# Optimization experiments

Measured on AMD Instinct MI355X. Metric: run time of the kernel, lower is better.

The kernel has to match this reference:

```python
import jax, jax.numpy as jnp
import numpy as np

B, T, C = 2, 2048, 2048
NH, NKV = 16, 4
HD = C // NH  # 128


def _rope(x, cos, sin):
    d = x.shape[-1] // 2
    x1, x2 = x[..., :d], x[..., d:]
    return jnp.concatenate([x1 * cos + x2 * sin, -x1 * sin + x2 * cos], axis=-1)


def _rmsnorm(x):
    eps = jnp.finfo(x.dtype).eps
    return x * jax.lax.rsqrt(jnp.mean(jnp.square(x), axis=-1, keepdims=True) + eps)


def setup_inputs() -> dict:
    key = jax.random.key(0)
    ks = jax.random.split(key, 7)
    s = 0.02
    return {
        "x": jax.random.normal(ks[0], (B, T, C), jnp.float32),
        "cos": jax.random.normal(ks[1], (1, T, 1, HD // 2), jnp.float32),
        "sin": jax.random.normal(ks[2], (1, T, 1, HD // 2), jnp.float32),
        "wq": jax.random.normal(ks[3], (C, NH * HD), jnp.float32) * s,
        "wk": jax.random.normal(ks[4], (C, NKV * HD), jnp.float32) * s,
        "wv": jax.random.normal(ks[5], (C, NKV * HD), jnp.float32) * s,
        "wo": jax.random.normal(ks[6], (C, C), jnp.float32) * s,
    }


def reference(x, cos, sin, wq, wk, wv, wo):
    q = (x @ wq).reshape(B, T, NH, HD)
    k = (x @ wk).reshape(B, T, NKV, HD)
    v = (x @ wv).reshape(B, T, NKV, HD)
    q = _rmsnorm(_rope(q, cos, sin))
    k = _rmsnorm(_rope(k, cos, sin))
    # [B, H, T, D]
    q = q.transpose(0, 2, 1, 3)
    k = k.transpose(0, 2, 1, 3)
    v = v.transpose(0, 2, 1, 3)
    rep = NH // NKV
    k = jnp.repeat(k, rep, axis=1)
    v = jnp.repeat(v, rep, axis=1)
    scale = 1.0 / jnp.sqrt(jnp.float32(HD))
    scores = jnp.einsum("bhqd,bhkd->bhqk", q, k) * scale
    causal = jnp.tril(jnp.ones((T, T), bool))
    scores = jnp.where(causal, scores, jnp.finfo(scores.dtype).min)
    attn = jax.nn.softmax(scores, axis=-1)
    y = jnp.einsum("bhqk,bhkd->bhqd", attn, v)
    y = y.transpose(0, 2, 1, 3).reshape(B, T, C)
    return y @ wo
```

## Files before the change

### kernel.cpp

```cpp
#include <hip/hip_runtime.h>
#include <hip/hip_bf16.h>
#include <cstdint>

typedef unsigned short u16;
typedef __bf16 bf16x8 __attribute__((ext_vector_type(8)));
typedef float f32x4 __attribute__((ext_vector_type(4)));
typedef unsigned short u16x4 __attribute__((ext_vector_type(4)));
typedef unsigned short u16x8 __attribute__((ext_vector_type(8)));
typedef unsigned uint2v __attribute__((ext_vector_type(2)));

#define B_ 2
#define T_ 2048
#define C_ 2048
#define NH_ 16
#define NKV_ 4
#define HD_ 128
#define K2_ 0.12752004650581538f

__device__ __forceinline__ u16 f2bf(float f) {
    unsigned u = __builtin_bit_cast(unsigned, f);
    unsigned r = u + 0x7FFFu + ((u >> 16) & 1u);
    return (u16)(r >> 16);
}

__device__ __forceinline__ float bf2f(u16 v) {
    unsigned u = ((unsigned)v) << 16;
    return __builtin_bit_cast(float, u);
}

__device__ __forceinline__ unsigned cvtpk(float a, float b) {
    unsigned r;
    asm("v_cvt_pk_bf16_f32 %0, %1, %2" : "=v"(r) : "v"(a), "v"(b));
    return r;
}

__device__ __forceinline__ void gl16(const void* g, void* l) {
    auto gp = reinterpret_cast<const __attribute__((address_space(1))) unsigned*>(
        reinterpret_cast<uintptr_t>(g));
    auto lp = reinterpret_cast<__attribute__((address_space(3))) unsigned*>(
        reinterpret_cast<uintptr_t>(l));
    __builtin_amdgcn_global_load_lds(gp, lp, 16, 0, 0);
}

__global__ void transpose_conv(const float* __restrict__ in, u16* __restrict__ out, int N) {
    __shared__ float tile[32][33];
    int n0 = blockIdx.x * 32, k0 = blockIdx.y * 32;
    int tx = threadIdx.x, ty = threadIdx.y;
#pragma unroll
    for (int i = 0; i < 4; ++i)
        tile[ty * 4 + i][tx] = in[(size_t)(k0 + ty * 4 + i) * N + n0 + tx];
    __syncthreads();
#pragma unroll
    for (int i = 0; i < 4; ++i)
        out[(size_t)(n0 + ty * 4 + i) * 2048 + k0 + tx] = f2bf(tile[tx][ty * 4 + i]);
}

__global__ void convert4(const float4* __restrict__ in, u16* __restrict__ out) {
    int i = blockIdx.x * 256 + threadIdx.x;
    float4 v = in[i];
    u16x4 o;
    o[0] = f2bf(v.x); o[1] = f2bf(v.y); o[2] = f2bf(v.z); o[3] = f2bf(v.w);
    ((u16x4*)out)[i] = o;
}

__global__ __launch_bounds__(256, 2) void gemm_bf16(const u16* __restrict__ A,
                                                    const u16* __restrict__ BT,
                                                    float* __restrict__ C, int N, int K) {
    __shared__ __align__(16) u16 As[2][128 * 64];
    __shared__ __align__(16) u16 Bs[2][128 * 64];
    int nwg = gridDim.x * gridDim.y;
    int bid = blockIdx.y * gridDim.x + blockIdx.x;
    int nb = (bid & 7) * (nwg >> 3) + (bid >> 3);
    int bx = nb % gridDim.x, by = nb / gridDim.x;

    int t = threadIdx.x;
    int w = t >> 6, l = t & 63;
    int wr = w >> 1, wc = w & 1;
    int lg = l >> 4, lr = l & 15;
    int m0 = by * 128, n0 = bx * 128;
    f32x4 acc[4][4] = {};

    size_t goff[4];
#pragma unroll
    for (int i = 0; i < 4; ++i) {
        int g = t + i * 256;
        goff[i] = (size_t)(g >> 3) * K * 2 + (size_t)(((g & 7) ^ ((g >> 3) & 7)) * 16);
    }
    const char* Ab = (const char*)A + (size_t)m0 * K * 2;
    const char* Bb = (const char*)BT + (size_t)n0 * K * 2;

    auto stage = [&](int kt, int buf) {
        char* Ad = (char*)As[buf] + t * 16;
        char* Bd = (char*)Bs[buf] + t * 16;
#pragma unroll
        for (int i = 0; i < 4; ++i) {
            gl16(Ab + (size_t)kt * 2 + goff[i], Ad + i * 4096);
            gl16(Bb + (size_t)kt * 2 + goff[i], Bd + i * 4096);
        }
    };

    stage(0, 0);
    int nk = K >> 6;
    for (int ki = 0; ki < nk; ++ki) {
        asm volatile("s_waitcnt vmcnt(0)" ::: "memory");
        __builtin_amdgcn_s_barrier();
        __builtin_amdgcn_sched_barrier(0);
        int cur = ki & 1;
        if (ki + 1 < nk) stage((ki + 1) * 64, cur ^ 1);
#pragma unroll
        for (int kk = 0; kk < 2; ++kk) {
            bf16x8 af[4], bfr[4];
#pragma unroll
            for (int m = 0; m < 4; ++m)
                af[m] = *(const bf16x8*)&As[cur][(wr * 64 + m * 16 + lr) * 64 +
                                                (((kk * 4 + lg) ^ (lr & 7)) * 8)];
#pragma unroll
            for (int n = 0; n < 4; ++n)
                bfr[n] = *(const bf16x8*)&Bs[cur][(wc * 64 + n * 16 + lr) * 64 +
                                                 (((kk * 4 + lg) ^ (lr & 7)) * 8)];
#pragma unroll
            for (int m = 0; m < 4; ++m)
#pragma unroll
                for (int n = 0; n < 4; ++n)
                    acc[m][n] = __builtin_amdgcn_mfma_f32_16x16x32_bf16(af[m], bfr[n], acc[m][n], 0, 0, 0);
        }
    }
#pragma unroll
    for (int m = 0; m < 4; ++m) {
        int row = m0 + wr * 64 + m * 16 + lg * 4;
#pragma unroll
        for (int n = 0; n < 4; ++n) {
            int col = n0 + wc * 64 + n * 16 + lr;
            float* Cp = C + (size_t)row * N + col;
#pragma unroll
            for (int r = 0; r < 4; ++r)
                Cp[(size_t)r * N] = acc[m][n][r];
        }
    }
}

__global__ __launch_bounds__(256, 2) void gemm_bf16o(const u16* __restrict__ A,
                                                     const u16* __restrict__ BT,
                                                     u16* __restrict__ C, int N, int K) {
    __shared__ __align__(16) u16 As[2][128 * 64];
    __shared__ __align__(16) u16 Bs[2][128 * 64];
    int nwg = gridDim.x * gridDim.y;
    int bid = blockIdx.y * gridDim.x + blockIdx.x;
    int nb = (bid & 7) * (nwg >> 3) + (bid >> 3);
    int bx = nb % gridDim.x, by = nb / gridDim.x;

    int t = threadIdx.x;
    int w = t >> 6, l = t & 63;
    int wr = w >> 1, wc = w & 1;
    int lg = l >> 4, lr = l & 15;
    int m0 = by * 128, n0 = bx * 128;
    f32x4 acc[4][4] = {};

    size_t goff[4];
#pragma unroll
    for (int i = 0; i < 4; ++i) {
        int g = t + i * 256;
        goff[i] = (size_t)(g >> 3) * K * 2 + (size_t)(((g & 7) ^ ((g >> 3) & 7)) * 16);
    }
    const char* Ab = (const char*)A + (size_t)m0 * K * 2;
    const char* Bb = (const char*)BT + (size_t)n0 * K * 2;

    auto stage = [&](int kt, int buf) {
        char* Ad = (char*)As[buf] + t * 16;
        char* Bd = (char*)Bs[buf] + t * 16;
#pragma unroll
        for (int i = 0; i < 4; ++i) {
            gl16(Ab + (size_t)kt * 2 + goff[i], Ad + i * 4096);
            gl16(Bb + (size_t)kt * 2 + goff[i], Bd + i * 4096);
        }
    };

    stage(0, 0);
    int nk = K >> 6;
    for (int ki = 0; ki < nk; ++ki) {
        asm volatile("s_waitcnt vmcnt(0)" ::: "memory");
        __builtin_amdgcn_s_barrier();
        __builtin_amdgcn_sched_barrier(0);
        int cur = ki & 1;
        if (ki + 1 < nk) stage((ki + 1) * 64, cur ^ 1);
#pragma unroll
        for (int kk = 0; kk < 2; ++kk) {
            bf16x8 af[4], bfr[4];
#pragma unroll
            for (int m = 0; m < 4; ++m)
                af[m] = *(const bf16x8*)&As[cur][(wr * 64 + m * 16 + lr) * 64 +
                                                (((kk * 4 + lg) ^ (lr & 7)) * 8)];
#pragma unroll
            for (int n = 0; n < 4; ++n)
                bfr[n] = *(const bf16x8*)&Bs[cur][(wc * 64 + n * 16 + lr) * 64 +
                                                 (((kk * 4 + lg) ^ (lr & 7)) * 8)];
#pragma unroll
            for (int m = 0; m < 4; ++m)
#pragma unroll
                for (int n = 0; n < 4; ++n)
                    acc[m][n] = __builtin_amdgcn_mfma_f32_16x16x32_bf16(af[m], bfr[n], acc[m][n], 0, 0, 0);
        }
    }
#pragma unroll
    for (int m = 0; m < 4; ++m) {
        int row = m0 + wr * 64 + m * 16 + lg * 4;
#pragma unroll
        for (int n = 0; n < 4; ++n) {
            int col = n0 + wc * 64 + n * 16 + lr;
            u16* Cp = C + (size_t)row * N + col;
#pragma unroll
            for (int r = 0; r < 4; ++r)
                Cp[(size_t)r * N] = f2bf(acc[m][n][r]);
        }
    }
}

__global__ void rope_rms(const u16* __restrict__ qkv, const float* __restrict__ cs,
                         const float* __restrict__ sn, u16* __restrict__ qh,
                         u16* __restrict__ kh) {
    int task = blockIdx.x * 4 + (threadIdx.x >> 6);
    int l = threadIdx.x & 63;
    const u16* in;
    u16* out;
    int tpos;
    float post = 1.0f;
    if (task < 65536) {
        int row = task >> 4, h = task & 15;
        in = qkv + (size_t)row * 3072 + h * 128;
        int b = row >> 11; tpos = row & 2047;
        out = qh + ((size_t)(b * NH_ + h) * T_ + tpos) * HD_;
        post = K2_;
    } else {
        int t2 = task - 65536;
        int row = t2 >> 2, h = t2 & 3;
        in = qkv + (size_t)row * 3072 + 2048 + h * 128;
        int b = row >> 11; tpos = row & 2047;
        out = kh + ((size_t)(b * NKV_ + h) * T_ + tpos) * HD_;
    }
    float x1 = bf2f(in[l]), x2 = bf2f(in[l + 64]);
    float c = cs[tpos * 64 + l], s = sn[tpos * 64 + l];
    float o1 = x1 * c + x2 * s;
    float o2 = -x1 * s + x2 * c;
    float ss = o1 * o1 + o2 * o2;
#pragma unroll
    for (int m = 1; m < 64; m <<= 1) ss += __shfl_xor(ss, m);
    float r = rsqrtf(ss * (1.0f / 128.0f) + 1.1920929e-07f) * post;
    out[l] = f2bf(o1 * r);
    out[l + 64] = f2bf(o2 * r);
}

__global__ void transpose_v(const u16* __restrict__ qkv, u16* __restrict__ vt) {
    __shared__ u16 tile[32][34];
    int t0 = blockIdx.x * 32;
    int d0 = blockIdx.y * 32;
    int bk = blockIdx.z;
    int b = bk >> 2, kvh = bk & 3;
    int tx = threadIdx.x, ty = threadIdx.y;
#pragma unroll
    for (int i = 0; i < 4; ++i)
        tile[ty * 4 + i][tx] =
            qkv[(size_t)(b * 2048 + t0 + ty * 4 + i) * 3072 + 2560 + kvh * 128 + d0 + tx];
    __syncthreads();
#pragma unroll
    for (int i = 0; i < 4; ++i)
        vt[((size_t)bk * 128 + d0 + ty * 4 + i) * 2048 + t0 + tx] = tile[tx][ty * 4 + i];
}

__global__ __launch_bounds__(256, 2) void attn(const u16* __restrict__ Q,
                                               const u16* __restrict__ Kk,
                                               const u16* __restrict__ V,
                                               u16* __restrict__ Y,
                                               u16* __restrict__ Opart,
                                               float2* __restrict__ Ml) {
    extern __shared__ __align__(16) u16 sm[];
    u16* Ks = sm;
    u16* Vs = sm + 16384;
    u16* Pb = sm + 24576;

    int bid = blockIdx.x;
    int xcd = bid & 7;
    int b = xcd >> 2, kvh = xcd & 3;
    int tidx = bid >> 3;
    int j, g0, g1, seg;
    bool split;
    if (tidx < 32) {
        j = tidx; g0 = 0; g1 = (j >> 1) + 1; split = false; seg = 0;
    } else if (tidx < 64) {
        j = 95 - tidx; int NNs = (j >> 1) + 1;
        g0 = 0; g1 = NNs >> 1; split = true; seg = 0;
    } else {
        j = 127 - tidx; int NNs = (j >> 1) + 1;
        g0 = NNs >> 1; g1 = NNs; split = true; seg = 1;
    }
    int t = threadIdx.x;
    int w = t >> 6, l = t & 63;
    int lg = l >> 4, lr = l & 15;
    int h = kvh * 4 + w;
    int qw = j * 32;

    const u16* Qp = Q + (size_t)(b * NH_ + h) * T_ * HD_;
    const u16* Kp = Kk + (size_t)(b * NKV_ + kvh) * T_ * HD_;
    const u16* Vp = V + (size_t)(b * NKV_ + kvh) * HD_ * T_;
    u16* Yp = Y + (size_t)(b * T_) * 2048 + h * HD_;
    u16* Pw = Pb + w * 512;

    size_t koff[4], voff[4];
#pragma unroll
    for (int i = 0; i < 4; ++i) {
        int g = t + i * 256;
        koff[i] = (size_t)(g >> 4) * 256 + (size_t)(((g & 15) ^ ((g >> 4) & 15)) * 16);
        voff[i] = (size_t)(g >> 3) * (T_ * 2) + (size_t)(((g & 7) ^ ((g >> 3) & 7)) * 16);
    }
    auto stageK = [&](int kv0, int buf) {
        const char* Kb = (const char*)Kp + (size_t)kv0 * 256;
        char* Kd = (char*)Ks + buf * 16384 + t * 16;
#pragma unroll
        for (int i = 0; i < 4; ++i) gl16(Kb + koff[i], Kd + i * 4096);
    };
    auto stageV = [&](int kv0) {
        const char* Vb = (const char*)Vp + (size_t)kv0 * 2;
        char* Vd = (char*)Vs + t * 16;
#pragma unroll
        for (int i = 0; i < 4; ++i) gl16(Vb + voff[i], Vd + i * 4096);
    };

    bf16x8 aq[2][4];
#pragma unroll
    for (int qf = 0; qf < 2; ++qf)
#pragma unroll
        for (int ch = 0; ch < 4; ++ch)
            aq[qf][ch] = *(const bf16x8*)(Qp + (size_t)(qw + qf * 16 + lr) * HD_ + ch * 32 + lg * 8);

    f32x4 acc[2][8] = {};
    float m2[2] = {-1e30f, -1e30f};
    float lp_[2] = {0.0f, 0.0f};

    stageK(g0 * 64, 0);

    for (int gi = g0; gi < g1; ++gi) {
        asm volatile("s_waitcnt vmcnt(0)" ::: "memory");
        __builtin_amdgcn_s_barrier();
        __builtin_amdgcn_sched_barrier(0);
        int cur = (gi - g0) & 1;
        int kv0 = gi * 64;
        stageV(kv0);
        __builtin_amdgcn_sched_barrier(0);
        int gn = (gi + 1 < g1) ? gi + 1 : g0;
        stageK(gn * 64, cur ^ 1);
        __builtin_amdgcn_sched_barrier(0);
        int kbase = cur * 8192;

        f32x4 sc[2][4] = {};
        __builtin_amdgcn_s_setprio(1);
#pragma unroll
        for (int ch = 0; ch < 4; ++ch)
#pragma unroll
            for (int kf = 0; kf < 4; ++kf) {
                bf16x8 bk = *(const bf16x8*)&Ks[kbase + (kf * 16 + lr) * 128 + (((ch * 4 + lg) ^ lr) * 8)];
                sc[0][kf] = __builtin_amdgcn_mfma_f32_16x16x32_bf16(bk, aq[0][ch], sc[0][kf], 0, 0, 0);
                sc[1][kf] = __builtin_amdgcn_mfma_f32_16x16x32_bf16(bk, aq[1][ch], sc[1][kf], 0, 0, 0);
            }
        __builtin_amdgcn_s_setprio(0);

        if (kv0 + 63 > qw) {
#pragma unroll
            for (int qf = 0; qf < 2; ++qf) {
                int qrow = qw + qf * 16 + lr;
#pragma unroll
                for (int kf = 0; kf < 4; ++kf)
#pragma unroll
                    for (int r = 0; r < 4; ++r) {
                        int key = kv0 + kf * 16 + 4 * lg + r;
                        if (key > qrow) sc[qf][kf][r] = -1e38f;
                    }
            }
        }
        float mx[2];
#pragma unroll
        for (int qf = 0; qf < 2; ++qf) {
            float m = sc[qf][0][0];
#pragma unroll
            for (int kf = 0; kf < 4; ++kf)
#pragma unroll
                for (int r = 0; r < 4; ++r) m = fmaxf(m, sc[qf][kf][r]);
            m = fmaxf(m, __shfl_xor(m, 16));
            m = fmaxf(m, __shfl_xor(m, 32));
            mx[qf] = m;
        }
        bool upd = (mx[0] > m2[0] + 8.0f) || (mx[1] > m2[1] + 8.0f);
        if (__any(upd)) {
#pragma unroll
            for (int qf = 0; qf < 2; ++qf) {
                float mn = fmaxf(m2[qf], mx[qf]);
                float rs = exp2f(m2[qf] - mn);
                m2[qf] = mn;
                lp_[qf] *= rs;
                float rs4[4];
#pragma unroll
                for (int r = 0; r < 4; ++r) rs4[r] = __shfl(rs, 4 * lg + r, 16);
#pragma unroll
                for (int oc = 0; oc < 8; ++oc)
#pragma unroll
                    for (int r = 0; r < 4; ++r) acc[qf][oc][r] *= rs4[r];
            }
        }
        bf16x8 ap[2][2];
#pragma unroll
        for (int kk = 0; kk < 2; ++kk) {
#pragma unroll
            for (int qf = 0; qf < 2; ++qf) {
                float ps = 0.0f;
#pragma unroll
                for (int kfl = 0; kfl < 2; ++kfl) {
                    int kf = kk * 2 + kfl;
                    float p0 = exp2f(sc[qf][kf][0] - m2[qf]);
                    float p1 = exp2f(sc[qf][kf][1] - m2[qf]);
                    float p2 = exp2f(sc[qf][kf][2] - m2[qf]);
                    float p3 = exp2f(sc[qf][kf][3] - m2[qf]);
                    ps += (p0 + p1) + (p2 + p3);
                    uint2v pk;
                    pk[0] = cvtpk(p0, p1);
                    pk[1] = cvtpk(p2, p3);
                    int g = 2 * kfl + (lg >> 1);
                    *(uint2v*)&Pw[lr * 32 + ((g ^ (lr & 3)) * 8) + (lg & 1) * 4] = pk;
                }
                lp_[qf] += ps;
                ap[qf][kk] = *(const bf16x8*)&Pw[lr * 32 + ((lg ^ (lr & 3)) * 8)];
            }
        }
        asm volatile("s_waitcnt vmcnt(4)" ::: "memory");
        __builtin_amdgcn_s_barrier();
        __builtin_amdgcn_sched_barrier(0);

        __builtin_amdgcn_s_setprio(1);
#pragma unroll
        for (int oc = 0; oc < 8; ++oc)
#pragma unroll
            for (int kk = 0; kk < 2; ++kk) {
                bf16x8 bv = *(const bf16x8*)&Vs[(oc * 16 + lr) * 64 +
                                                (((kk * 4 + lg) ^ (lr & 7)) * 8)];
                acc[0][oc] = __builtin_amdgcn_mfma_f32_16x16x32_bf16(ap[0][kk], bv, acc[0][oc], 0, 0, 0);
                acc[1][oc] = __builtin_amdgcn_mfma_f32_16x16x32_bf16(ap[1][kk], bv, acc[1][oc], 0, 0, 0);
            }
        __builtin_amdgcn_s_setprio(0);
    }
    asm volatile("s_waitcnt vmcnt(0)" ::: "memory");

    float ltr[2];
#pragma unroll
    for (int qf = 0; qf < 2; ++qf) {
        float lt = lp_[qf];
        lt += __shfl_xor(lt, 16);
        lt += __shfl_xor(lt, 32);
        ltr[qf] = lt;
    }

    if (!split) {
#pragma unroll
        for (int qf = 0; qf < 2; ++qf) {
            float inv = 1.0f / ltr[qf];
            float inv4[4];
#pragma unroll
            for (int r = 0; r < 4; ++r) inv4[r] = __shfl(inv, 4 * lg + r, 16);
#pragma unroll
            for (int oc = 0; oc < 8; ++oc)
#pragma unroll
                for (int r = 0; r < 4; ++r)
                    Yp[(size_t)(qw + qf * 16 + 4 * lg + r) * 2048 + oc * 16 + lr] =
                        f2bf(acc[qf][oc][r] * inv4[r]);
        }
    } else {
        int s32 = j - 32;
        size_t pbase = (((size_t)(xcd * 32 + s32) * 2 + seg) * 4 + w);
        u16* Op = Opart + pbase * 4096;
        float2* mlp = Ml + pbase * 32;
#pragma unroll
        for (int qf = 0; qf < 2; ++qf)
#pragma unroll
            for (int oc = 0; oc < 8; ++oc)
#pragma unroll
                for (int r = 0; r < 4; ++r)
                    Op[(qf * 16 + 4 * lg + r) * 128 + oc * 16 + lr] = f2bf(acc[qf][oc][r]);
        if (lg == 0) {
            mlp[lr] = float2{m2[0], ltr[0]};
            mlp[16 + lr] = float2{m2[1], ltr[1]};
        }
    }
}

__global__ __launch_bounds__(256) void combine(const u16* __restrict__ Opart,
                                               const float2* __restrict__ Ml,
                                               u16* __restrict__ Y) {
    int blk = blockIdx.x;
    int w = blk & 3;
    int s32 = (blk >> 2) & 31;
    int xcd = blk >> 7;
    int b = xcd >> 2, kvh = xcd & 3, h = kvh * 4 + w;
    int qw = (32 + s32) * 32;
    size_t p0 = (((size_t)(xcd * 32 + s32) * 2 + 0) * 4 + w);
    size_t p1 = (((size_t)(xcd * 32 + s32) * 2 + 1) * 4 + w);
    int t = threadIdx.x;
    int row = t >> 3, c0 = (t & 7) * 16;
    float2 a = Ml[p0 * 32 + row];
    float2 c = Ml[p1 * 32 + row];
    float M = fmaxf(a.x, c.x);
    float w1 = exp2f(a.x - M), w2 = exp2f(c.x - M);
    float inv = 1.0f / (w1 * a.y + w2 * c.y);
    const u16* O1 = Opart + p0 * 4096 + row * 128 + c0;
    const u16* O2 = Opart + p1 * 4096 + row * 128 + c0;
    u16* Yp = Y + ((size_t)(b * T_) + qw + row) * 2048 + h * HD_ + c0;
    u16x8 v1a = *(const u16x8*)O1, v1b = *(const u16x8*)(O1 + 8);
    u16x8 v2a = *(const u16x8*)O2, v2b = *(const u16x8*)(O2 + 8);
    u16x8 oa, ob;
#pragma unroll
    for (int i = 0; i < 8; ++i) {
        oa[i] = f2bf((w1 * bf2f(v1a[i]) + w2 * bf2f(v2a[i])) * inv);
        ob[i] = f2bf((w1 * bf2f(v1b[i]) + w2 * bf2f(v2b[i])) * inv);
    }
    *(u16x8*)Yp = oa;
    *(u16x8*)(Yp + 8) = ob;
}

extern "C" void kernel_launch(void* const* d_in, const int* in_sizes, int n_in,
                              void* d_out, int out_size, void* d_ws, size_t ws_size,
                              hipStream_t stream) {
    const float* x    = (const float*)d_in[0];
    const float* cosT = (const float*)d_in[1];
    const float* sinT = (const float*)d_in[2];
    const float* wq   = (const float*)d_in[3];
    const float* wk   = (const float*)d_in[4];
    const float* wv   = (const float*)d_in[5];
    const float* wo   = (const float*)d_in[6];
    float* out = (float*)d_out;

    char* ws = (char*)d_ws;
    u16*    wqkvT = (u16*)(ws);
    u16*    woT   = (u16*)(ws + 12582912);
    u16*    xb    = (u16*)(ws + 20971520);
    u16*    qkv   = (u16*)(ws + 37748736);
    u16*    opart = (u16*)(ws + 62914560);
    float2* mlbuf = (float2*)(ws + 79691776);
    u16*    qh    = (u16*)(ws + 88080384);
    u16*    kh    = (u16*)(ws + 104857600);
    u16*    vt    = (u16*)(ws + 109051904);
    u16*    y     = xb;

    hipFuncSetAttribute(reinterpret_cast<const void*>(&attn),
                        hipFuncAttributeMaxDynamicSharedMemorySize, 53248);

    transpose_conv<<<dim3(64, 64), dim3(32, 8), 0, stream>>>(wq, wqkvT, 2048);
    transpose_conv<<<dim3(16, 64), dim3(32, 8), 0, stream>>>(wk, wqkvT + (size_t)2048 * 2048, 512);
    transpose_conv<<<dim3(16, 64), dim3(32, 8), 0, stream>>>(wv, wqkvT + (size_t)2560 * 2048, 512);
    transpose_conv<<<dim3(64, 64), dim3(32, 8), 0, stream>>>(wo, woT, 2048);
    convert4<<<8192, 256, 0, stream>>>((const float4*)x, xb);

    gemm_bf16o<<<dim3(24, 32), 256, 0, stream>>>(xb, wqkvT, qkv, 3072, 2048);

    rope_rms<<<20480, 256, 0, stream>>>(qkv, cosT, sinT, qh, kh);
    transpose_v<<<dim3(64, 4, 8), dim3(32, 8), 0, stream>>>(qkv, vt);

    attn<<<768, 256, 53248, stream>>>(qh, kh, vt, y, opart, mlbuf);
    combine<<<1024, 256, 0, stream>>>(opart, mlbuf, y);

    gemm_bf16<<<dim3(16, 32), 256, 0, stream>>>(y, woT, out, 2048, 2048);
}
```

Before: 201.9 us.

## Widen attention blocks to 512 threads covering 64 query rows per KV tile

The attention kernel now uses 8 waves per block, two query sub-tiles of 32 rows for each of the 4 heads. Each staged K/V tile is therefore shared by twice as many queries, which halves the global-to-LDS traffic per query. The split-KV schedule and the combine kernel are remapped to match: 16 unsplit tiles, 32 split halves, and combine reading 64-row partials. In exchange, occupancy drops to one block per CU, with larger blocks, fewer of them, and coarser load balancing.

```diff
diff --git a/kernel.cpp b/kernel.cpp
--- a/kernel.cpp
+++ b/kernel.cpp
@@ -266,7 +266,7 @@
         vt[((size_t)bk * 128 + d0 + ty * 4 + i) * 2048 + t0 + tx] = tile[tx][ty * 4 + i];
 }
 
-__global__ __launch_bounds__(256, 2) void attn(const u16* __restrict__ Q,
+__global__ __launch_bounds__(512, 1) void attn(const u16* __restrict__ Q,
                                                const u16* __restrict__ Kk,
                                                const u16* __restrict__ V,
                                                u16* __restrict__ Y,
@@ -280,23 +280,22 @@
     int bid = blockIdx.x;
     int xcd = bid & 7;
     int b = xcd >> 2, kvh = xcd & 3;
-    int tidx = bid >> 3;
+    int tk = bid >> 3;
     int j, g0, g1, seg;
     bool split;
-    if (tidx < 32) {
-        j = tidx; g0 = 0; g1 = (j >> 1) + 1; split = false; seg = 0;
-    } else if (tidx < 64) {
-        j = 95 - tidx; int NNs = (j >> 1) + 1;
-        g0 = 0; g1 = NNs >> 1; split = true; seg = 0;
+    if (tk < 16) {
+        j = tk; g0 = 0; g1 = j + 1; split = false; seg = 0;
+    } else if (tk < 32) {
+        j = tk; g0 = 0; g1 = 16; split = true; seg = 0;
     } else {
-        j = 127 - tidx; int NNs = (j >> 1) + 1;
-        g0 = NNs >> 1; g1 = NNs; split = true; seg = 1;
+        j = 63 - tk; g0 = 16; g1 = j + 1; split = true; seg = 1;
     }
     int t = threadIdx.x;
     int w = t >> 6, l = t & 63;
     int lg = l >> 4, lr = l & 15;
-    int h = kvh * 4 + w;
-    int qw = j * 32;
+    int hh = w & 3;
+    int h = kvh * 4 + hh;
+    int qw = j * 64 + (w >> 2) * 32;
 
     const u16* Qp = Q + (size_t)(b * NH_ + h) * T_ * HD_;
     const u16* Kp = Kk + (size_t)(b * NKV_ + kvh) * T_ * HD_;
@@ -304,10 +303,10 @@
     u16* Yp = Y + (size_t)(b * T_) * 2048 + h * HD_;
     u16* Pw = Pb + w * 512;
 
-    size_t koff[4], voff[4];
-#pragma unroll
-    for (int i = 0; i < 4; ++i) {
-        int g = t + i * 256;
+    size_t koff[2], voff[2];
+#pragma unroll
+    for (int i = 0; i < 2; ++i) {
+        int g = t + i * 512;
         koff[i] = (size_t)(g >> 4) * 256 + (size_t)(((g & 15) ^ ((g >> 4) & 15)) * 16);
         voff[i] = (size_t)(g >> 3) * (T_ * 2) + (size_t)(((g & 7) ^ ((g >> 3) & 7)) * 16);
     }
@@ -315,13 +314,13 @@
         const char* Kb = (const char*)Kp + (size_t)kv0 * 256;
         char* Kd = (char*)Ks + buf * 16384 + t * 16;
 #pragma unroll
-        for (int i = 0; i < 4; ++i) gl16(Kb + koff[i], Kd + i * 4096);
+        for (int i = 0; i < 2; ++i) gl16(Kb + koff[i], Kd + i * 8192);
     };
     auto stageV = [&](int kv0) {
         const char* Vb = (const char*)Vp + (size_t)kv0 * 2;
         char* Vd = (char*)Vs + t * 16;
 #pragma unroll
-        for (int i = 0; i < 4; ++i) gl16(Vb + voff[i], Vd + i * 4096);
+        for (int i = 0; i < 2; ++i) gl16(Vb + voff[i], Vd + i * 8192);
     };
 
     bf16x8 aq[2][4];
@@ -428,7 +427,7 @@
                 ap[qf][kk] = *(const bf16x8*)&Pw[lr * 32 + ((lg ^ (lr & 3)) * 8)];
             }
         }
-        asm volatile("s_waitcnt vmcnt(4)" ::: "memory");
+        asm volatile("s_waitcnt vmcnt(2)" ::: "memory");
         __builtin_amdgcn_s_barrier();
         __builtin_amdgcn_sched_barrier(0);
 
@@ -470,20 +469,21 @@
                         f2bf(acc[qf][oc][r] * inv4[r]);
         }
     } else {
-        int s32 = j - 32;
-        size_t pbase = (((size_t)(xcd * 32 + s32) * 2 + seg) * 4 + w);
-        u16* Op = Opart + pbase * 4096;
-        float2* mlp = Ml + pbase * 32;
+        int s16 = j - 16;
+        size_t pbase = (((size_t)(xcd * 16 + s16) * 4 + hh) * 2 + seg);
+        u16* Op = Opart + pbase * 8192;
+        float2* mlp = Ml + pbase * 64;
+        int ro = (w >> 2) * 32;
 #pragma unroll
         for (int qf = 0; qf < 2; ++qf)
 #pragma unroll
             for (int oc = 0; oc < 8; ++oc)
 #pragma unroll
                 for (int r = 0; r < 4; ++r)
-                    Op[(qf * 16 + 4 * lg + r) * 128 + oc * 16 + lr] = f2bf(acc[qf][oc][r]);
+                    Op[(ro + qf * 16 + 4 * lg + r) * 128 + oc * 16 + lr] = f2bf(acc[qf][oc][r]);
         if (lg == 0) {
-            mlp[lr] = float2{m2[0], ltr[0]};
-            mlp[16 + lr] = float2{m2[1], ltr[1]};
+            mlp[ro + lr] = float2{m2[0], ltr[0]};
+            mlp[ro + 16 + lr] = float2{m2[1], ltr[1]};
         }
     }
 }
@@ -492,33 +492,33 @@
                                                const float2* __restrict__ Ml,
                                                u16* __restrict__ Y) {
     int blk = blockIdx.x;
-    int w = blk & 3;
-    int s32 = (blk >> 2) & 31;
-    int xcd = blk >> 7;
-    int b = xcd >> 2, kvh = xcd & 3, h = kvh * 4 + w;
-    int qw = (32 + s32) * 32;
-    size_t p0 = (((size_t)(xcd * 32 + s32) * 2 + 0) * 4 + w);
-    size_t p1 = (((size_t)(xcd * 32 + s32) * 2 + 1) * 4 + w);
+    int hh = blk & 3;
+    int s16 = (blk >> 2) & 15;
+    int xcd = blk >> 6;
+    int b = xcd >> 2, kvh = xcd & 3, h = kvh * 4 + hh;
+    size_t p0 = (size_t)blk * 2;
+    size_t p1 = p0 + 1;
     int t = threadIdx.x;
-    int row = t >> 3, c0 = (t & 7) * 16;
-    float2 a = Ml[p0 * 32 + row];
-    float2 c = Ml[p1 * 32 + row];
+    int row = t >> 2, c0 = (t & 3) * 32;
+    float2 a = Ml[p0 * 64 + row];
+    float2 c = Ml[p1 * 64 + row];
     float M = fmaxf(a.x, c.x);
     float w1 = exp2f(a.x - M), w2 = exp2f(c.x - M);
     float inv = 1.0f / (w1 * a.y + w2 * c.y);
-    const u16* O1 = Opart + p0 * 4096 + row * 128 + c0;
-    const u16* O2 = Opart + p1 * 4096 + row * 128 + c0;
-    u16* Yp = Y + ((size_t)(b * T_) + qw + row) * 2048 + h * HD_ + c0;
-    u16x8 v1a = *(const u16x8*)O1, v1b = *(const u16x8*)(O1 + 8);
-    u16x8 v2a = *(const u16x8*)O2, v2b = *(const u16x8*)(O2 + 8);
-    u16x8 oa, ob;
-#pragma unroll
-    for (int i = 0; i < 8; ++i) {
-        oa[i] = f2bf((w1 * bf2f(v1a[i]) + w2 * bf2f(v2a[i])) * inv);
-        ob[i] = f2bf((w1 * bf2f(v1b[i]) + w2 * bf2f(v2b[i])) * inv);
-    }
-    *(u16x8*)Yp = oa;
-    *(u16x8*)(Yp + 8) = ob;
+    const u16* O1 = Opart + p0 * 8192 + row * 128 + c0;
+    const u16* O2 = Opart + p1 * 8192 + row * 128 + c0;
+    int qrow = (16 + s16) * 64 + row;
+    u16* Yp = Y + ((size_t)(b * T_) + qrow) * 2048 + h * HD_ + c0;
+#pragma unroll
+    for (int v = 0; v < 4; ++v) {
+        u16x8 v1 = *(const u16x8*)(O1 + v * 8);
+        u16x8 v2 = *(const u16x8*)(O2 + v * 8);
+        u16x8 o;
+#pragma unroll
+        for (int i = 0; i < 8; ++i)
+            o[i] = f2bf((w1 * bf2f(v1[i]) + w2 * bf2f(v2[i])) * inv);
+        *(u16x8*)(Yp + v * 8) = o;
+    }
 }
 
 extern "C" void kernel_launch(void* const* d_in, const int* in_sizes, int n_in,
@@ -546,7 +546,7 @@
     u16*    y     = xb;
 
     hipFuncSetAttribute(reinterpret_cast<const void*>(&attn),
-                        hipFuncAttributeMaxDynamicSharedMemorySize, 53248);
+                        hipFuncAttributeMaxDynamicSharedMemorySize, 57344);
 
     transpose_conv<<<dim3(64, 64), dim3(32, 8), 0, stream>>>(wq, wqkvT, 2048);
     transpose_conv<<<dim3(16, 64), dim3(32, 8), 0, stream>>>(wk, wqkvT + (size_t)2048 * 2048, 512);
@@ -559,8 +559,8 @@
     rope_rms<<<20480, 256, 0, stream>>>(qkv, cosT, sinT, qh, kh);
     transpose_v<<<dim3(64, 4, 8), dim3(32, 8), 0, stream>>>(qkv, vt);
 
-    attn<<<768, 256, 53248, stream>>>(qh, kh, vt, y, opart, mlbuf);
-    combine<<<1024, 256, 0, stream>>>(opart, mlbuf, y);
+    attn<<<384, 512, 57344, stream>>>(qh, kh, vt, y, opart, mlbuf);
+    combine<<<512, 256, 0, stream>>>(opart, mlbuf, y);
 
     gemm_bf16<<<dim3(16, 32), 256, 0, stream>>>(y, woT, out, 2048, 2048);
 }
```

Result: no change. 200.9 us (-0.5%).

## Merge prep kernels and single-buffer attention K/V to fit three blocks per CU

Applied to the files above, without the earlier changes.

Folds the four weight transpose-converts and the x conversion into one prepass launch, and rope_rms with transpose_v into one launch, which cuts kernel launch count. In attention, K staging drops from double to single buffering, shrinking LDS from 52KB to 36KB so launch bounds can rise to three blocks per CU. K and V are now loaded together at the top of each iteration and waited on in full, so load latency is no longer prefetched behind compute and must be hidden by the extra occupancy instead.

```diff
diff --git a/kernel.cpp b/kernel.cpp
--- a/kernel.cpp
+++ b/kernel.cpp
@@ -42,10 +42,34 @@
     __builtin_amdgcn_global_load_lds(gp, lp, 16, 0, 0);
 }
 
-__global__ void transpose_conv(const float* __restrict__ in, u16* __restrict__ out, int N) {
+__global__ __launch_bounds__(256) void prepass(const float* __restrict__ wq,
+                                               const float* __restrict__ wk,
+                                               const float* __restrict__ wv,
+                                               const float* __restrict__ wo,
+                                               const float4* __restrict__ x,
+                                               u16* __restrict__ wqkvT,
+                                               u16* __restrict__ woT,
+                                               u16* __restrict__ xb) {
+    int bz = blockIdx.x;
+    int t = threadIdx.x;
+    if (bz >= 10240) {
+        int i = (bz - 10240) * 256 + t;
+        float4 v = x[i];
+        u16x4 o;
+        o[0] = f2bf(v.x); o[1] = f2bf(v.y); o[2] = f2bf(v.z); o[3] = f2bf(v.w);
+        ((u16x4*)xb)[i] = o;
+        return;
+    }
     __shared__ float tile[32][33];
-    int n0 = blockIdx.x * 32, k0 = blockIdx.y * 32;
-    int tx = threadIdx.x, ty = threadIdx.y;
+    const float* in;
+    u16* out;
+    int N, bx, by;
+    if (bz < 4096)      { in = wq; out = wqkvT;                      N = 2048; bx = bz & 63; by = bz >> 6; }
+    else if (bz < 5120) { int z = bz - 4096; in = wk; out = wqkvT + (size_t)2048 * 2048; N = 512; bx = z & 15; by = z >> 4; }
+    else if (bz < 6144) { int z = bz - 5120; in = wv; out = wqkvT + (size_t)2560 * 2048; N = 512; bx = z & 15; by = z >> 4; }
+    else                { int z = bz - 6144; in = wo; out = woT;     N = 2048; bx = z & 63; by = z >> 6; }
+    int n0 = bx * 32, k0 = by * 32;
+    int tx = t & 31, ty = t >> 5;
 #pragma unroll
     for (int i = 0; i < 4; ++i)
         tile[ty * 4 + i][tx] = in[(size_t)(k0 + ty * 4 + i) * N + n0 + tx];
@@ -53,14 +77,6 @@
 #pragma unroll
     for (int i = 0; i < 4; ++i)
         out[(size_t)(n0 + ty * 4 + i) * 2048 + k0 + tx] = f2bf(tile[tx][ty * 4 + i]);
-}
-
-__global__ void convert4(const float4* __restrict__ in, u16* __restrict__ out) {
-    int i = blockIdx.x * 256 + threadIdx.x;
-    float4 v = in[i];
-    u16x4 o;
-    o[0] = f2bf(v.x); o[1] = f2bf(v.y); o[2] = f2bf(v.z); o[3] = f2bf(v.w);
-    ((u16x4*)out)[i] = o;
 }
 
 __global__ __launch_bounds__(256, 2) void gemm_bf16(const u16* __restrict__ A,
@@ -215,47 +231,52 @@
     }
 }
 
-__global__ void rope_rms(const u16* __restrict__ qkv, const float* __restrict__ cs,
-                         const float* __restrict__ sn, u16* __restrict__ qh,
-                         u16* __restrict__ kh) {
-    int task = blockIdx.x * 4 + (threadIdx.x >> 6);
-    int l = threadIdx.x & 63;
-    const u16* in;
-    u16* out;
-    int tpos;
-    float post = 1.0f;
-    if (task < 65536) {
-        int row = task >> 4, h = task & 15;
-        in = qkv + (size_t)row * 3072 + h * 128;
-        int b = row >> 11; tpos = row & 2047;
-        out = qh + ((size_t)(b * NH_ + h) * T_ + tpos) * HD_;
-        post = K2_;
-    } else {
-        int t2 = task - 65536;
-        int row = t2 >> 2, h = t2 & 3;
-        in = qkv + (size_t)row * 3072 + 2048 + h * 128;
-        int b = row >> 11; tpos = row & 2047;
-        out = kh + ((size_t)(b * NKV_ + h) * T_ + tpos) * HD_;
-    }
-    float x1 = bf2f(in[l]), x2 = bf2f(in[l + 64]);
-    float c = cs[tpos * 64 + l], s = sn[tpos * 64 + l];
-    float o1 = x1 * c + x2 * s;
-    float o2 = -x1 * s + x2 * c;
-    float ss = o1 * o1 + o2 * o2;
-#pragma unroll
-    for (int m = 1; m < 64; m <<= 1) ss += __shfl_xor(ss, m);
-    float r = rsqrtf(ss * (1.0f / 128.0f) + 1.1920929e-07f) * post;
-    out[l] = f2bf(o1 * r);
-    out[l + 64] = f2bf(o2 * r);
-}
-
-__global__ void transpose_v(const u16* __restrict__ qkv, u16* __restrict__ vt) {
+__global__ __launch_bounds__(256) void rope_tv(const u16* __restrict__ qkv,
+                                               const float* __restrict__ cs,
+                                               const float* __restrict__ sn,
+                                               u16* __restrict__ qh, u16* __restrict__ kh,
+                                               u16* __restrict__ vt) {
+    int bz = blockIdx.x;
+    int t = threadIdx.x;
+    if (bz < 20480) {
+        int task = bz * 4 + (t >> 6);
+        int l = t & 63;
+        const u16* in;
+        u16* out;
+        int tpos;
+        float post = 1.0f;
+        if (task < 65536) {
+            int row = task >> 4, h = task & 15;
+            in = qkv + (size_t)row * 3072 + h * 128;
+            int b = row >> 11; tpos = row & 2047;
+            out = qh + ((size_t)(b * NH_ + h) * T_ + tpos) * HD_;
+            post = K2_;
+        } else {
+            int t2 = task - 65536;
+            int row = t2 >> 2, h = t2 & 3;
+            in = qkv + (size_t)row * 3072 + 2048 + h * 128;
+            int b = row >> 11; tpos = row & 2047;
+            out = kh + ((size_t)(b * NKV_ + h) * T_ + tpos) * HD_;
+        }
+        float x1 = bf2f(in[l]), x2 = bf2f(in[l + 64]);
+        float c = cs[tpos * 64 + l], s = sn[tpos * 64 + l];
+        float o1 = x1 * c + x2 * s;
+        float o2 = -x1 * s + x2 * c;
+        float ss = o1 * o1 + o2 * o2;
+#pragma unroll
+        for (int m = 1; m < 64; m <<= 1) ss += __shfl_xor(ss, m);
+        float r = rsqrtf(ss * (1.0f / 128.0f) + 1.1920929e-07f) * post;
+        out[l] = f2bf(o1 * r);
+        out[l + 64] = f2bf(o2 * r);
+        return;
+    }
     __shared__ u16 tile[32][34];
-    int t0 = blockIdx.x * 32;
-    int d0 = blockIdx.y * 32;
-    int bk = blockIdx.z;
+    int z = bz - 20480;
+    int t0 = (z & 63) * 32;
+    int d0 = ((z >> 6) & 3) * 32;
+    int bk = z >> 8;
     int b = bk >> 2, kvh = bk & 3;
-    int tx = threadIdx.x, ty = threadIdx.y;
+    int tx = t & 31, ty = t >> 5;
 #pragma unroll
     for (int i = 0; i < 4; ++i)
         tile[ty * 4 + i][tx] =
@@ -266,7 +287,7 @@
         vt[((size_t)bk * 128 + d0 + ty * 4 + i) * 2048 + t0 + tx] = tile[tx][ty * 4 + i];
 }
 
-__global__ __launch_bounds__(256, 2) void attn(const u16* __restrict__ Q,
+__global__ __launch_bounds__(256, 3) void attn(const u16* __restrict__ Q,
                                                const u16* __restrict__ Kk,
                                                const u16* __restrict__ V,
                                                u16* __restrict__ Y,
@@ -274,8 +295,8 @@
                                                float2* __restrict__ Ml) {
     extern __shared__ __align__(16) u16 sm[];
     u16* Ks = sm;
-    u16* Vs = sm + 16384;
-    u16* Pb = sm + 24576;
+    u16* Vs = sm + 8192;
+    u16* Pb = sm + 16384;
 
     int bid = blockIdx.x;
     int xcd = bid & 7;
@@ -311,18 +332,6 @@
         koff[i] = (size_t)(g >> 4) * 256 + (size_t)(((g & 15) ^ ((g >> 4) & 15)) * 16);
         voff[i] = (size_t)(g >> 3) * (T_ * 2) + (size_t)(((g & 7) ^ ((g >> 3) & 7)) * 16);
     }
-    auto stageK = [&](int kv0, int buf) {
-        const char* Kb = (const char*)Kp + (size_t)kv0 * 256;
-        char* Kd = (char*)Ks + buf * 16384 + t * 16;
-#pragma unroll
-        for (int i = 0; i < 4; ++i) gl16(Kb + koff[i], Kd + i * 4096);
-    };
-    auto stageV = [&](int kv0) {
-        const char* Vb = (const char*)Vp + (size_t)kv0 * 2;
-        char* Vd = (char*)Vs + t * 16;
-#pragma unroll
-        for (int i = 0; i < 4; ++i) gl16(Vb + voff[i], Vd + i * 4096);
-    };
 
     bf16x8 aq[2][4];
 #pragma unroll
@@ -335,20 +344,23 @@
     float m2[2] = {-1e30f, -1e30f};
     float lp_[2] = {0.0f, 0.0f};
 
-    stageK(g0 * 64, 0);
-
     for (int gi = g0; gi < g1; ++gi) {
+        int kv0 = gi * 64;
+        __builtin_amdgcn_s_barrier();
+        {
+            const char* Kb = (const char*)Kp + (size_t)kv0 * 256;
+            const char* Vb = (const char*)Vp + (size_t)kv0 * 2;
+            char* Kd = (char*)Ks + t * 16;
+            char* Vd = (char*)Vs + t * 16;
+#pragma unroll
+            for (int i = 0; i < 4; ++i) {
+                gl16(Kb + koff[i], Kd + i * 4096);
+                gl16(Vb + voff[i], Vd + i * 4096);
+            }
+        }
         asm volatile("s_waitcnt vmcnt(0)" ::: "memory");
         __builtin_amdgcn_s_barrier();
         __builtin_amdgcn_sched_barrier(0);
-        int cur = (gi - g0) & 1;
-        int kv0 = gi * 64;
-        stageV(kv0);
-        __builtin_amdgcn_sched_barrier(0);
-        int gn = (gi + 1 < g1) ? gi + 1 : g0;
-        stageK(gn * 64, cur ^ 1);
-        __builtin_amdgcn_sched_barrier(0);
-        int kbase = cur * 8192;
 
         f32x4 sc[2][4] = {};
         __builtin_amdgcn_s_setprio(1);
@@ -356,7 +368,7 @@
         for (int ch = 0; ch < 4; ++ch)
 #pragma unroll
             for (int kf = 0; kf < 4; ++kf) {
-                bf16x8 bk = *(const bf16x8*)&Ks[kbase + (kf * 16 + lr) * 128 + (((ch * 4 + lg) ^ lr) * 8)];
+                bf16x8 bk = *(const bf16x8*)&Ks[(kf * 16 + lr) * 128 + (((ch * 4 + lg) ^ lr) * 8)];
                 sc[0][kf] = __builtin_amdgcn_mfma_f32_16x16x32_bf16(bk, aq[0][ch], sc[0][kf], 0, 0, 0);
                 sc[1][kf] = __builtin_amdgcn_mfma_f32_16x16x32_bf16(bk, aq[1][ch], sc[1][kf], 0, 0, 0);
             }
@@ -428,10 +440,6 @@
                 ap[qf][kk] = *(const bf16x8*)&Pw[lr * 32 + ((lg ^ (lr & 3)) * 8)];
             }
         }
-        asm volatile("s_waitcnt vmcnt(4)" ::: "memory");
-        __builtin_amdgcn_s_barrier();
-        __builtin_amdgcn_sched_barrier(0);
-
         __builtin_amdgcn_s_setprio(1);
 #pragma unroll
         for (int oc = 0; oc < 8; ++oc)
@@ -444,7 +452,6 @@
             }
         __builtin_amdgcn_s_setprio(0);
     }
-    asm volatile("s_waitcnt vmcnt(0)" ::: "memory");
 
     float ltr[2];
 #pragma unroll
@@ -546,20 +553,15 @@
     u16*    y     = xb;
 
     hipFuncSetAttribute(reinterpret_cast<const void*>(&attn),
-                        hipFuncAttributeMaxDynamicSharedMemorySize, 53248);
-
-    transpose_conv<<<dim3(64, 64), dim3(32, 8), 0, stream>>>(wq, wqkvT, 2048);
-    transpose_conv<<<dim3(16, 64), dim3(32, 8), 0, stream>>>(wk, wqkvT + (size_t)2048 * 2048, 512);
-    transpose_conv<<<dim3(16, 64), dim3(32, 8), 0, stream>>>(wv, wqkvT + (size_t)2560 * 2048, 512);
-    transpose_conv<<<dim3(64, 64), dim3(32, 8), 0, stream>>>(wo, woT, 2048);
-    convert4<<<8192, 256, 0, stream>>>((const float4*)x, xb);
+                        hipFuncAttributeMaxDynamicSharedMemorySize, 36864);
+
+    prepass<<<18432, 256, 0, stream>>>(wq, wk, wv, wo, (const float4*)x, wqkvT, woT, xb);
 
     gemm_bf16o<<<dim3(24, 32), 256, 0, stream>>>(xb, wqkvT, qkv, 3072, 2048);
 
-    rope_rms<<<20480, 256, 0, stream>>>(qkv, cosT, sinT, qh, kh);
-    transpose_v<<<dim3(64, 4, 8), dim3(32, 8), 0, stream>>>(qkv, vt);
-
-    attn<<<768, 256, 53248, stream>>>(qh, kh, vt, y, opart, mlbuf);
+    rope_tv<<<22528, 256, 0, stream>>>(qkv, cosT, sinT, qh, kh, vt);
+
+    attn<<<768, 256, 36864, stream>>>(qh, kh, vt, y, opart, mlbuf);
     combine<<<1024, 256, 0, stream>>>(opart, mlbuf, y);
 
     gemm_bf16<<<dim3(16, 32), 256, 0, stream>>>(y, woT, out, 2048, 2048);
```

Result: slower. 219.8 us (+8.8%).
